# Kernel tuning notes

Hardware: AMD Instinct MI355X
Metric: run time of the kernel (lower is better)

Reference implementation:

```python
import jax, jax.numpy as jnp
import numpy as np

N, E, F = 50000, 400000, 128
H0, C0 = 1, 128   # layer 0: heads=1, out=128 (concat=False -> mean over heads)
H1, C1 = 4, 64    # layer 1: heads=4, out=64
EPS_BN = 1e-5
NEG_SLOPE = 0.2


def setup_inputs() -> dict:
    key = jax.random.key(0)
    ks = jax.random.split(key, 12)

    def w(k, shape, fan_in):
        return jax.random.normal(k, shape, jnp.float32) / np.float32(np.sqrt(fan_in))

    return {
        "emb": jax.random.normal(ks[0], (N, F), jnp.float32),
        "edge_weight": jax.random.uniform(ks[1], (E,), jnp.float32),
        # GATv2Conv layer 0 params (lin_l, lin_r, lin_edge, att, out bias)
        "Wl0": w(ks[2], (F, H0 * C0), F), "bl0": jnp.zeros((H0 * C0,), jnp.float32),
        "Wr0": w(ks[3], (F, H0 * C0), F), "br0": jnp.zeros((H0 * C0,), jnp.float32),
        "We0": w(ks[4], (1, H0 * C0), 1), "att0": w(ks[5], (H0, C0), C0),
        "b0": jnp.zeros((C0,), jnp.float32),
        "g0": jnp.ones((C0,), jnp.float32), "be0": jnp.zeros((C0,), jnp.float32),
        # GATv2Conv layer 1 params
        "Wl1": w(ks[6], (C0, H1 * C1), C0), "bl1": jnp.zeros((H1 * C1,), jnp.float32),
        "Wr1": w(ks[7], (C0, H1 * C1), C0), "br1": jnp.zeros((H1 * C1,), jnp.float32),
        "We1": w(ks[8], (1, H1 * C1), 1), "att1": w(ks[9], (H1, C1), C1),
        "b1": jnp.zeros((C1,), jnp.float32),
        "g1": jnp.ones((C1,), jnp.float32), "be1": jnp.zeros((C1,), jnp.float32),
        "edge_index": jax.random.randint(ks[10], (2, E), 0, N, jnp.int32),
    }


def gatv2(x, src, dst, ea, Wl, bl, Wr, br, We, att, b, H, C):
    """PyG GATv2Conv, edge_dim=1, concat=False (mean over heads), eval dropout."""
    n = x.shape[0]
    xl = (x @ Wl + bl).reshape(n, H, C)
    xr = (x @ Wr + br).reshape(n, H, C)
    ef = (ea[:, None] @ We).reshape(-1, H, C)           # [Et,H,C] edge embedding
    m = jax.nn.leaky_relu(xl[src] + xr[dst] + ef, NEG_SLOPE)  # [Et,H,C]
    alpha = jnp.einsum('ehc,hc->eh', m, att)            # attention logits
    amax = jax.ops.segment_max(alpha, dst, num_segments=n)
    ex = jnp.exp(alpha - amax[dst])
    den = jax.ops.segment_sum(ex, dst, num_segments=n)
    a = ex / (den[dst] + 1e-16)                          # segment softmax (PyG eps)
    out = jax.ops.segment_sum(a[:, :, None] * xl[src], dst, num_segments=n)
    return out.mean(axis=1) + b                          # concat=False -> head mean


def batchnorm(x, g, be):
    mu = x.mean(0)
    v = x.var(0)  # biased variance, as torch BN uses for normalization
    return g * (x - mu) * jax.lax.rsqrt(v + EPS_BN) + be


def _forward(emb, edge_weight, Wl0, bl0, Wr0, br0, We0, att0, b0, g0, be0,
             Wl1, bl1, Wr1, br1, We1, att1, b1, g1, be1, edge_index):
    loop = jnp.arange(N, dtype=edge_index.dtype)
    src = jnp.concatenate([edge_index[0], loop])
    dst = jnp.concatenate([edge_index[1], loop])
    # add_self_loops with fill_value='mean' for edge_attr
    ea = jnp.concatenate([edge_weight, jnp.full((N,), edge_weight.mean(), edge_weight.dtype)])
    # NOTE: zip(layer_stack, batchnorm_stack) truncates -> only first 2 of 3 GAT
    # layers execute, each followed by BN + ELU (+ identity dropout, p=0).
    h = gatv2(emb, src, dst, ea, Wl0, bl0, Wr0, br0, We0, att0, b0, H0, C0)
    h = jax.nn.elu(batchnorm(h, g0, be0))
    h = gatv2(h, src, dst, ea, Wl1, bl1, Wr1, br1, We1, att1, b1, H1, C1)
    h = jax.nn.elu(batchnorm(h, g1, be1))
    return h


def reference(emb, edge_weight, Wl0, bl0, Wr0, br0, We0, att0, b0, g0, be0,
              Wl1, bl1, Wr1, br1, We1, att1, b1, g1, be1, edge_index):
    return _forward(emb, edge_weight, Wl0, bl0, Wr0, br0, We0, att0, b0, g0, be0,
                    Wl1, bl1, Wr1, br1, We1, att1, b1, g1, be1, edge_index)
```

## Files before the change

### kernel.cpp

```cpp
#include <hip/hip_runtime.h>
#include <cstdint>
#include <cstddef>
#include <type_traits>

using f32x4 = __attribute__((ext_vector_type(4))) float;
using s16x8 = __attribute__((ext_vector_type(8))) short;

__device__ __forceinline__ ushort f2bf(float x) {
    uint32_t u = __builtin_bit_cast(uint32_t, x);
    u += 0x7fffu + ((u >> 16) & 1u);
    return (ushort)(u >> 16);
}
__device__ __forceinline__ float bflo(uint32_t u) { return __builtin_bit_cast(float, u << 16); }
__device__ __forceinline__ float bfhi(uint32_t u) { return __builtin_bit_cast(float, u & 0xffff0000u); }

__device__ __forceinline__ void dec8(uint4 g, float* x) {
    x[0] = bflo(g.x); x[1] = bfhi(g.x); x[2] = bflo(g.y); x[3] = bfhi(g.y);
    x[4] = bflo(g.z); x[5] = bfhi(g.z); x[6] = bflo(g.w); x[7] = bfhi(g.w);
}

#define GLOAD_LDS16(g, l)                                                                  \
    __builtin_amdgcn_global_load_lds((const __attribute__((address_space(1))) void*)(g),  \
                                     (__attribute__((address_space(3))) void*)(l), 16, 0, 0)

__global__ __launch_bounds__(256) void degree_ew_wt(const int* __restrict__ ei,
                                                    const float* __restrict__ ew,
                                                    int* __restrict__ deg,
                                                    float* __restrict__ partials,
                                                    int E, int N, int NBE,
                                                    const float* __restrict__ Wl0,
                                                    const float* __restrict__ Wr0,
                                                    ushort* __restrict__ WT0,
                                                    const float* __restrict__ Wl1,
                                                    const float* __restrict__ Wr1,
                                                    ushort* __restrict__ WT1) {
    __shared__ float red[256];
    int bid = blockIdx.x;
    int t = threadIdx.x;
    if (bid < NBE) {
        int e = bid * 256 + t;
        float s = (e < E) ? ew[e] : 0.f;
        red[t] = s; __syncthreads();
        for (int o = 128; o; o >>= 1) { if (t < o) red[t] += red[t + o]; __syncthreads(); }
        if (t == 0) partials[bid] = red[0];
        if (e < E + N) {
            int d = (e < E) ? ei[E + e] : (e - E);
            atomicAdd(&deg[d], 1);
        }
        return;
    }
    int j = (bid - NBE) * 256 + t;
    if (j < 128 * 256) {
        int k = j >> 8, c = j & 255;
        float v = (c < 128) ? Wl0[k * 128 + c] : Wr0[k * 128 + (c - 128)];
        WT0[(size_t)c * 128 + k] = f2bf(v);
        return;
    }
    j -= 128 * 256;
    if (j < 128 * 512) {
        int k = j >> 9, c = j & 511;
        float v = (c < 256) ? Wl1[k * 256 + c] : Wr1[k * 256 + (c - 256)];
        WT1[(size_t)c * 128 + k] = f2bf(v);
    }
}

__global__ void scan_partial(const int* __restrict__ deg, int n, int* __restrict__ bsum) {
    __shared__ int lds[256];
    int t = threadIdx.x;
    int base = blockIdx.x * 1024 + t * 4;
    int s = 0;
#pragma unroll
    for (int j = 0; j < 4; ++j) if (base + j < n) s += deg[base + j];
    lds[t] = s; __syncthreads();
    for (int o = 128; o; o >>= 1) { if (t < o) lds[t] += lds[t + o]; __syncthreads(); }
    if (t == 0) bsum[blockIdx.x] = lds[0];
}

__global__ void scan_block(const int* __restrict__ bsum, int nb, int* __restrict__ boff,
                           int* __restrict__ row_start, int n, int total,
                           const float* __restrict__ partials, int nbp, int E,
                           float* __restrict__ stats) {
    __shared__ int lds[256];
    __shared__ float fred[256];
    int t = threadIdx.x;
    int v = (t < nb) ? bsum[t] : 0;
    lds[t] = v; __syncthreads();
    for (int o = 1; o < 256; o <<= 1) {
        int y = (t >= o) ? lds[t - o] : 0;
        __syncthreads();
        lds[t] += y;
        __syncthreads();
    }
    if (t < nb) boff[t] = lds[t] - v;
    if (t == 0) row_start[n] = total;
    stats[t] = 0.f; stats[256 + t] = 0.f;
    float fs = 0.f;
    for (int j = t; j < nbp; j += 256) fs += partials[j];
    fred[t] = fs; __syncthreads();
    for (int o = 128; o; o >>= 1) { if (t < o) fred[t] += fred[t + o]; __syncthreads(); }
    if (t == 0) stats[0] = fred[0] / (float)E;
}

__global__ void scan_final(const int* __restrict__ deg, int n, const int* __restrict__ boff,
                           int* __restrict__ row_start, int* __restrict__ cursor) {
    __shared__ int lds[256];
    int t = threadIdx.x;
    int base = blockIdx.x * 1024 + t * 4;
    int d[4], loc[4], s = 0;
#pragma unroll
    for (int j = 0; j < 4; ++j) d[j] = (base + j < n) ? deg[base + j] : 0;
#pragma unroll
    for (int j = 0; j < 4; ++j) { loc[j] = s; s += d[j]; }
    lds[t] = s; __syncthreads();
    for (int o = 1; o < 256; o <<= 1) {
        int y = (t >= o) ? lds[t - o] : 0;
        __syncthreads();
        lds[t] += y;
        __syncthreads();
    }
    int texcl = lds[t] - s + boff[blockIdx.x];
#pragma unroll
    for (int j = 0; j < 4; ++j)
        if (base + j < n) { row_start[base + j] = texcl + loc[j]; cursor[base + j] = 0; }
}

__global__ void scatter_kernel(const int* __restrict__ ei, const float* __restrict__ ew,
                               const float* __restrict__ ew_mean, const int* __restrict__ row_start,
                               int* __restrict__ cursor, int* __restrict__ csr_src,
                               float* __restrict__ csr_ea, int E, int N) {
    int e = blockIdx.x * blockDim.x + threadIdx.x;
    if (e >= E + N) return;
    int s, d; float w;
    if (e < E) { s = ei[e]; d = ei[E + e]; w = ew[e]; }
    else       { s = d = e - E;            w = ew_mean[0]; }
    int pos = row_start[d] + atomicAdd(&cursor[d], 1);
    csr_src[pos] = s;
    csr_ea[pos] = w;
}

template <int MODE>
__global__ __launch_bounds__(512) void mfma_linear3(const void* __restrict__ Xv,
                                                    const ushort* __restrict__ WT,
                                                    const float* __restrict__ bnsums,
                                                    const float* __restrict__ gamma,
                                                    const float* __restrict__ beta,
                                                    const float* __restrict__ bl,
                                                    const float* __restrict__ br,
                                                    ushort* __restrict__ xl,
                                                    ushort* __restrict__ xr,
                                                    int n, int HALF) {
    constexpr int LW = (MODE == 1) ? 2 : 1;
    __shared__ ushort sB[128 * 128];
    __shared__ ushort sA[128 * 128];
    const int tid = threadIdx.x;
    const int c0 = blockIdx.x * 128;
    const int ntiles = (n + 127) >> 7;

    {
        const ushort* src = WT + (size_t)c0 * 128;
#pragma unroll
        for (int it = 0; it < 4; ++it) {
            int f = tid + it * 512;
            int row = f >> 4, ch = f & 15;
            const ushort* g = src + (size_t)row * 128 + ((ch ^ (row & 7)) << 3);
            ushort* lp = sB + (((size_t)it * 512 + (tid & ~63)) << 3);
            GLOAD_LDS16(g, lp);
        }
    }

    const int myc = (tid & 15) * 8;
    const int row0 = tid >> 4;
    const int swc = (tid & 15) ^ (row0 & 7);
    float Af[8], Bf[8];
    if constexpr (MODE == 2) {
        float invn = 1.f / (float)n;
#pragma unroll
        for (int j = 0; j < 8; ++j) {
            float mu = bnsums[myc + j] * invn;
            float var = bnsums[128 + myc + j] * invn - mu * mu;
            float rs = rsqrtf(var + 1e-5f);
            Af[j] = gamma[myc + j] * rs;
            Bf[j] = beta[myc + j] - mu * Af[j];
        }
    }

    uint4 rA[4][LW];
    auto loadA = [&](int rt) {
        int r0 = rt << 7;
#pragma unroll
        for (int it = 0; it < 4; ++it) {
            int gr = r0 + row0 + it * 32; gr = gr < n ? gr : n - 1;
            if constexpr (MODE == 1) {
                const float* src = (const float*)Xv + (size_t)gr * 128 + myc;
                rA[it][0] = *(const uint4*)src;
                rA[it][1] = *(const uint4*)(src + 4);
            } else {
                rA[it][0] = *(const uint4*)((const ushort*)Xv + (size_t)gr * 128 + myc);
            }
        }
    };
    auto writeA = [&]() {
#pragma unroll
        for (int it = 0; it < 4; ++it) {
            uint4 o;
            if constexpr (MODE == 0) {
                o = rA[it][0];
            } else if constexpr (MODE == 1) {
                float x[8] = {
                    __builtin_bit_cast(float, rA[it][0].x), __builtin_bit_cast(float, rA[it][0].y),
                    __builtin_bit_cast(float, rA[it][0].z), __builtin_bit_cast(float, rA[it][0].w),
                    __builtin_bit_cast(float, rA[it][1].x), __builtin_bit_cast(float, rA[it][1].y),
                    __builtin_bit_cast(float, rA[it][1].z), __builtin_bit_cast(float, rA[it][1].w)};
                ushort h[8];
#pragma unroll
                for (int j = 0; j < 8; ++j) h[j] = f2bf(x[j]);
                o.x = h[0] | ((uint32_t)h[1] << 16); o.y = h[2] | ((uint32_t)h[3] << 16);
                o.z = h[4] | ((uint32_t)h[5] << 16); o.w = h[6] | ((uint32_t)h[7] << 16);
            } else {
                float x[8]; dec8(rA[it][0], x);
                ushort h[8];
#pragma unroll
                for (int j = 0; j < 8; ++j) {
                    float v = fmaf(x[j], Af[j], Bf[j]);
                    v = v > 0.f ? v : __expf(v) - 1.f;
                    h[j] = f2bf(v);
                }
                o.x = h[0] | ((uint32_t)h[1] << 16); o.y = h[2] | ((uint32_t)h[3] << 16);
                o.z = h[4] | ((uint32_t)h[5] << 16); o.w = h[6] | ((uint32_t)h[7] << 16);
            }
            *(uint4*)&sA[(row0 + it * 32) * 128 + swc * 8] = o;
        }
    };

    const int w = tid >> 6, l = tid & 63, lr = l & 15, lg = l >> 4;
    const bool left = c0 < HALF;
    const float* bias = left ? bl : br;
    ushort* dst = left ? xl : xr;
    const int cb = left ? c0 : c0 - HALF;
    float bv[8];
#pragma unroll
    for (int tn = 0; tn < 8; ++tn) bv[tn] = bias[cb + tn * 16 + lr];
    const int arow = w * 16 + lr;

    int rt = blockIdx.y;
    loadA(rt);
    writeA();
    __syncthreads();

    while (true) {
        int nx = rt + gridDim.y;
        if (nx < ntiles) loadA(nx);

        f32x4 acc[8] = {};
#pragma unroll
        for (int kk = 0; kk < 4; ++kk) {
            int ach = (kk * 4 + lg) ^ (arow & 7);
            s16x8 a = *(const s16x8*)&sA[arow * 128 + (ach << 3)];
#pragma unroll
            for (int tn = 0; tn < 8; ++tn) {
                int brow = tn * 16 + lr;
                int bch = (kk * 4 + lg) ^ (brow & 7);
                s16x8 b = *(const s16x8*)&sB[brow * 128 + (bch << 3)];
                acc[tn] = __builtin_amdgcn_mfma_f32_16x16x32_bf16(a, b, acc[tn], 0, 0, 0);
            }
        }
        int rbase = (rt << 7) + w * 16 + lg * 4;
#pragma unroll
        for (int tn = 0; tn < 8; ++tn) {
            int colh = cb + tn * 16 + lr;
#pragma unroll
            for (int r = 0; r < 4; ++r) {
                int row = rbase + r;
                if (row < n) dst[(size_t)row * HALF + colh] = f2bf(acc[tn][r] + bv[tn]);
            }
        }
        if (nx >= ntiles) break;
        __syncthreads();
        writeA();
        __syncthreads();
        rt = nx;
    }
}

template <int H, int C, int LPN>
__global__ __launch_bounds__(256, 8) void gat_agg(const ushort* __restrict__ xl,
                                                  const ushort* __restrict__ xr,
                                                  const int* __restrict__ row_start,
                                                  const int* __restrict__ csr_src,
                                                  const float* __restrict__ csr_ea,
                                                  const float* __restrict__ We,
                                                  const float* __restrict__ att,
                                                  const float* __restrict__ bias,
                                                  ushort* __restrict__ out, int n) {
    constexpr int HC = H * C;
    constexpr int VPL = HC / LPN;
    constexpr int REDW = LPN / H;
    constexpr int NPW = 64 / LPN;
    static_assert(VPL == 8, "");

    const int wid = threadIdx.x >> 6;
    const int lane = threadIdx.x & 63;
    const int sl = lane & (LPN - 1);
    const int sub = lane / LPN;
    const int v = (blockIdx.x * 4 + wid) * NPW + sub;
    const bool valid = v < n;
    const int vv = valid ? v : n - 1;

    const int base = sl * VPL;
    const int e0 = row_start[vv];
    const int e1 = valid ? row_start[vv + 1] : row_start[vv + 1];

    uint4 gN; float wN;
    {
        int s = csr_src[e0];
        wN = csr_ea[e0];
        gN = *(const uint4*)&xl[(size_t)s * HC + base];
    }

    float xrv[8], wE[8], attv[8];
    dec8(*(const uint4*)&xr[(size_t)vv * HC + base], xrv);
#pragma unroll
    for (int j = 0; j < 8; j += 4) {
        float4 a = *(const float4*)&We[base + j];
        wE[j] = a.x; wE[j + 1] = a.y; wE[j + 2] = a.z; wE[j + 3] = a.w;
        float4 b = *(const float4*)&att[base + j];
        attv[j] = b.x; attv[j + 1] = b.y; attv[j + 2] = b.z; attv[j + 3] = b.w;
    }

    float m, den, acc[8];
    {
        uint4 g = gN; float w = wN;
        if (e0 + 1 < e1) {
            int s = csr_src[e0 + 1];
            wN = csr_ea[e0 + 1];
            gN = *(const uint4*)&xl[(size_t)s * HC + base];
        }
        float xf[8];
        dec8(g, xf);
        float t1 = 0.f, t2 = 0.f;
#pragma unroll
        for (int j = 0; j < 8; ++j) {
            float u = xf[j] + fmaf(w, wE[j], xrv[j]);
            t1 = fmaf(u, attv[j], t1);
            t2 = fmaf(__builtin_fabsf(u), attv[j], t2);
        }
        float p = fmaf(0.6f, t1, 0.4f * t2);
#pragma unroll
        for (int o = REDW >> 1; o; o >>= 1) p += __shfl_xor(p, o, 64);
        m = p; den = 1.f;
#pragma unroll
        for (int j = 0; j < 8; ++j) acc[j] = xf[j];
    }

    for (int e = e0 + 1; e < e1; ++e) {
        uint4 g = gN; float w = wN;
        if (e + 1 < e1) {
            int s = csr_src[e + 1];
            wN = csr_ea[e + 1];
            gN = *(const uint4*)&xl[(size_t)s * HC + base];
        }
        float xf[8];
        dec8(g, xf);
        float t1 = 0.f, t2 = 0.f;
#pragma unroll
        for (int j = 0; j < 8; ++j) {
            float u = xf[j] + fmaf(w, wE[j], xrv[j]);
            t1 = fmaf(u, attv[j], t1);
            t2 = fmaf(__builtin_fabsf(u), attv[j], t2);
        }
        float p = fmaf(0.6f, t1, 0.4f * t2);
#pragma unroll
        for (int o = REDW >> 1; o; o >>= 1) p += __shfl_xor(p, o, 64);
        float dd = p - m;
        if (__builtin_expect(dd > 8.f, 0)) {
            float r = __expf(-dd);
            den = fmaf(den, r, 1.f);
#pragma unroll
            for (int j = 0; j < 8; ++j) acc[j] = fmaf(acc[j], r, xf[j]);
            m = p;
        } else {
            float pe = __expf(dd);
            den += pe;
#pragma unroll
            for (int j = 0; j < 8; ++j) acc[j] = fmaf(pe, xf[j], acc[j]);
        }
    }

    float inv = 1.f / den;
#pragma unroll
    for (int j = 0; j < 8; ++j) acc[j] *= inv;

    if constexpr (H > 1) {
#pragma unroll
        for (int o = REDW; o < LPN; o <<= 1)
#pragma unroll
            for (int j = 0; j < 8; ++j) acc[j] += __shfl_xor(acc[j], o, 64);
#pragma unroll
        for (int j = 0; j < 8; ++j) acc[j] *= (1.f / (float)H);
    }

    if (valid && sl < C / VPL) {
        float bv[8];
#pragma unroll
        for (int j = 0; j < 8; j += 4) {
            float4 b = *(const float4*)&bias[sl * VPL + j];
            bv[j] = b.x; bv[j + 1] = b.y; bv[j + 2] = b.z; bv[j + 3] = b.w;
        }
        uint4 o;
        o.x = (uint32_t)f2bf(acc[0] + bv[0]) | ((uint32_t)f2bf(acc[1] + bv[1]) << 16);
        o.y = (uint32_t)f2bf(acc[2] + bv[2]) | ((uint32_t)f2bf(acc[3] + bv[3]) << 16);
        o.z = (uint32_t)f2bf(acc[4] + bv[4]) | ((uint32_t)f2bf(acc[5] + bv[5]) << 16);
        o.w = (uint32_t)f2bf(acc[6] + bv[6]) | ((uint32_t)f2bf(acc[7] + bv[7]) << 16);
        *(uint4*)&out[(size_t)v * C + sl * VPL] = o;
    }
}

template <int C>
__global__ __launch_bounds__(256) void bn_stats_bf16(const ushort* __restrict__ x, int n,
                                                     float* __restrict__ sums) {
    constexpr int C2 = C / 2;
    constexpr int RPB = 256 / C2;
    __shared__ float red[256];
    int t = threadIdx.x;
    int c2 = t % C2, rs = t / C2;
    float s0 = 0.f, s1 = 0.f, q0 = 0.f, q1 = 0.f;
    for (int row = blockIdx.x * RPB + rs; row < n; row += gridDim.x * RPB) {
        uint32_t u = *(const uint32_t*)&x[(size_t)row * C + c2 * 2];
        float a = bflo(u), b = bfhi(u);
        s0 += a; q0 += a * a; s1 += b; q1 += b * b;
    }
    float vals[4] = {s0, s1, q0, q1};
    float outv[4];
#pragma unroll
    for (int k = 0; k < 4; ++k) {
        red[t] = vals[k]; __syncthreads();
        if (rs == 0) {
            float s = red[c2];
#pragma unroll
            for (int r = 1; r < RPB; ++r) s += red[c2 + r * C2];
            outv[k] = s;
        }
        __syncthreads();
    }
    if (rs == 0) {
        atomicAdd(&sums[c2 * 2],     outv[0]);
        atomicAdd(&sums[c2 * 2 + 1], outv[1]);
        atomicAdd(&sums[C + c2 * 2],     outv[2]);
        atomicAdd(&sums[C + c2 * 2 + 1], outv[3]);
    }
}

template <int C>
__global__ __launch_bounds__(256) void bn_apply_elu_f32(const ushort* __restrict__ x, int n,
                                                        const float* __restrict__ g,
                                                        const float* __restrict__ be,
                                                        const float* __restrict__ sums,
                                                        float* __restrict__ outf) {
    int total = n * C / 8;
    float invn = 1.f / (float)n;
    for (int i = blockIdx.x * blockDim.x + threadIdx.x; i < total; i += gridDim.x * blockDim.x) {
        uint4 u = ((const uint4*)x)[i];
        int c0 = (i * 8) & (C - 1);
        float r[8] = {bflo(u.x), bfhi(u.x), bflo(u.y), bfhi(u.y),
                      bflo(u.z), bfhi(u.z), bflo(u.w), bfhi(u.w)};
#pragma unroll
        for (int j = 0; j < 8; ++j) {
            int c = c0 + j;
            float mu = sums[c] * invn;
            float var = sums[C + c] * invn - mu * mu;
            float t = g[c] * (r[j] - mu) * rsqrtf(var + 1e-5f) + be[c];
            r[j] = t > 0.f ? t : expm1f(t);
        }
        ((float4*)outf)[i * 2]     = make_float4(r[0], r[1], r[2], r[3]);
        ((float4*)outf)[i * 2 + 1] = make_float4(r[4], r[5], r[6], r[7]);
    }
}

extern "C" void kernel_launch(void* const* d_in, const int* in_sizes, int n_in,
                              void* d_out, int out_size, void* d_ws, size_t ws_size,
                              hipStream_t stream) {
    const float* emb = (const float*)d_in[0];
    const float* ew  = (const float*)d_in[1];
    const float* Wl0 = (const float*)d_in[2];
    const float* bl0 = (const float*)d_in[3];
    const float* Wr0 = (const float*)d_in[4];
    const float* br0 = (const float*)d_in[5];
    const float* We0 = (const float*)d_in[6];
    const float* att0 = (const float*)d_in[7];
    const float* b0  = (const float*)d_in[8];
    const float* g0  = (const float*)d_in[9];
    const float* be0 = (const float*)d_in[10];
    const float* Wl1 = (const float*)d_in[11];
    const float* bl1 = (const float*)d_in[12];
    const float* Wr1 = (const float*)d_in[13];
    const float* br1 = (const float*)d_in[14];
    const float* We1 = (const float*)d_in[15];
    const float* att1 = (const float*)d_in[16];
    const float* b1  = (const float*)d_in[17];
    const float* g1  = (const float*)d_in[18];
    const float* be1 = (const float*)d_in[19];
    const int* ei    = (const int*)d_in[20];

    const int N = in_sizes[0] / 128;
    const int E = in_sizes[1];
    const int Et = E + N;
    float* out = (float*)d_out;

    char* w = (char*)d_ws;
    size_t off = 0;
    auto alloc = [&](size_t bytes) {
        void* p = w + off;
        off = (off + bytes + 255) & ~(size_t)255;
        return p;
    };
    ushort* xlb    = (ushort*)alloc((size_t)N * 256 * 2);
    ushort* xrb    = (ushort*)alloc((size_t)N * 256 * 2);
    ushort* h0b16  = (ushort*)alloc((size_t)N * 128 * 2);
    ushort* out16  = (ushort*)alloc((size_t)N * 64 * 2);
    ushort* WT0    = (ushort*)alloc((size_t)256 * 128 * 2);
    ushort* WT1    = (ushort*)alloc((size_t)512 * 128 * 2);
    int*   deg     = (int*)alloc((size_t)2 * N * 4);
    int*   cursor  = deg + N;
    int*   row_st  = (int*)alloc((size_t)(N + 1) * 4);
    int*   csr_src = (int*)alloc((size_t)Et * 4);
    float* csr_ea  = (float*)alloc((size_t)Et * 4);
    int*   bsum    = (int*)alloc(256 * 4);
    int*   boff    = (int*)alloc(256 * 4);
    float* partials= (float*)alloc(2048 * 4);
    float* stats   = (float*)alloc(512 * 4);
    float* ew_mean = stats;
    float* bn0     = stats + 64;
    float* bn1     = stats + 64 + 256;
    (void)ws_size; (void)n_in; (void)out_size;

    hipMemsetAsync(deg, 0, (size_t)N * 4, stream);

    const int NBE = (Et + 255) / 256;
    const int WTB = (128 * 256 + 128 * 512) / 256;
    degree_ew_wt<<<NBE + WTB, 256, 0, stream>>>(ei, ew, deg, partials, E, N, NBE,
                                                Wl0, Wr0, WT0, Wl1, Wr1, WT1);
    const int NB1 = (N + 1023) / 1024;
    scan_partial<<<NB1, 256, 0, stream>>>(deg, N, bsum);
    scan_block<<<1, 256, 0, stream>>>(bsum, NB1, boff, row_st, N, Et, partials, NBE, E, stats);
    scan_final<<<NB1, 256, 0, stream>>>(deg, N, boff, row_st, cursor);
    scatter_kernel<<<NBE, 256, 0, stream>>>(ei, ew, ew_mean, row_st, cursor,
                                            csr_src, csr_ea, E, N);

    const int ntiles = (N + 127) / 128;
    const int GR0 = ntiles < 128 ? ntiles : 128;
    const int GR1 = ntiles < 64 ? ntiles : 64;

    mfma_linear3<1><<<dim3(2, GR0), 512, 0, stream>>>(emb, WT0, nullptr, nullptr, nullptr,
                                                      bl0, br0, xlb, xrb, N, 128);
    gat_agg<1, 128, 16><<<(N + 15) / 16, 256, 0, stream>>>(xlb, xrb, row_st, csr_src, csr_ea,
                                                           We0, att0, b0, h0b16, N);
    bn_stats_bf16<128><<<128, 256, 0, stream>>>(h0b16, N, bn0);

    mfma_linear3<2><<<dim3(4, GR1), 512, 0, stream>>>(h0b16, WT1, bn0, g0, be0,
                                                      bl1, br1, xlb, xrb, N, 256);
    gat_agg<4, 64, 32><<<(N + 7) / 8, 256, 0, stream>>>(xlb, xrb, row_st, csr_src, csr_ea,
                                                        We1, att1, b1, out16, N);
    bn_stats_bf16<64><<<128, 256, 0, stream>>>(out16, N, bn1);
    bn_apply_elu_f32<64><<<1024, 256, 0, stream>>>(out16, N, g1, be1, bn1, out);
}
```

Before: 267.7 us.

## Unroll GAT aggregation by two edges with deeper prefetch and raise GEMM grid

The edge loop in gat_agg now handles two edges per iteration. It prefetches the next two neighbour rows, computes both logits together, and does one online-softmax rescale against their max. The aim is to keep more gather loads in flight and cut the serial dependency per edge. Launch bounds drop to 6 waves to leave room for the extra registers, which may lower occupancy. The linear GEMM grids grow to up to 256 row tiles, with an early return for surplus blocks.

```diff
diff --git a/kernel.cpp b/kernel.cpp
--- a/kernel.cpp
+++ b/kernel.cpp
@@ -243,6 +243,7 @@
     const int arow = w * 16 + lr;
 
     int rt = blockIdx.y;
+    if (rt >= ntiles) return;
     loadA(rt);
     writeA();
     __syncthreads();
@@ -283,7 +284,7 @@
 }
 
 template <int H, int C, int LPN>
-__global__ __launch_bounds__(256, 8) void gat_agg(const ushort* __restrict__ xl,
+__global__ __launch_bounds__(256, 6) void gat_agg(const ushort* __restrict__ xl,
                                                   const ushort* __restrict__ xr,
                                                   const int* __restrict__ row_start,
                                                   const int* __restrict__ csr_src,
@@ -308,13 +309,23 @@
 
     const int base = sl * VPL;
     const int e0 = row_start[vv];
-    const int e1 = valid ? row_start[vv + 1] : row_start[vv + 1];
-
-    uint4 gN; float wN;
+    const int e1 = row_start[vv + 1];
+    const ushort* xlb = xl + base;
+
+    uint4 gF; float wF;
     {
         int s = csr_src[e0];
-        wN = csr_ea[e0];
-        gN = *(const uint4*)&xl[(size_t)s * HC + base];
+        wF = csr_ea[e0];
+        gF = *(const uint4*)&xlb[(size_t)s * HC];
+    }
+    uint4 gA, gB; float wA, wB;
+    {
+        int ea = e0 + 1 < e1 ? e0 + 1 : e0;
+        int eb = e0 + 2 < e1 ? e0 + 2 : e0;
+        int sa = csr_src[ea]; wA = csr_ea[ea];
+        int sb = csr_src[eb]; wB = csr_ea[eb];
+        gA = *(const uint4*)&xlb[(size_t)sa * HC];
+        gB = *(const uint4*)&xlb[(size_t)sb * HC];
     }
 
     float xrv[8], wE[8], attv[8];
@@ -329,18 +340,12 @@
 
     float m, den, acc[8];
     {
-        uint4 g = gN; float w = wN;
-        if (e0 + 1 < e1) {
-            int s = csr_src[e0 + 1];
-            wN = csr_ea[e0 + 1];
-            gN = *(const uint4*)&xl[(size_t)s * HC + base];
-        }
         float xf[8];
-        dec8(g, xf);
+        dec8(gF, xf);
         float t1 = 0.f, t2 = 0.f;
 #pragma unroll
         for (int j = 0; j < 8; ++j) {
-            float u = xf[j] + fmaf(w, wE[j], xrv[j]);
+            float u = xf[j] + fmaf(wF, wE[j], xrv[j]);
             t1 = fmaf(u, attv[j], t1);
             t2 = fmaf(__builtin_fabsf(u), attv[j], t2);
         }
@@ -352,19 +357,59 @@
         for (int j = 0; j < 8; ++j) acc[j] = xf[j];
     }
 
-    for (int e = e0 + 1; e < e1; ++e) {
-        uint4 g = gN; float w = wN;
-        if (e + 1 < e1) {
-            int s = csr_src[e + 1];
-            wN = csr_ea[e + 1];
-            gN = *(const uint4*)&xl[(size_t)s * HC + base];
-        }
+    int e = e0 + 1;
+    while (e + 1 < e1) {
+        uint4 g0 = gA, g1 = gB; float w0 = wA, w1 = wB;
+        {
+            int ea = e + 2 < e1 ? e + 2 : e;
+            int eb = e + 3 < e1 ? e + 3 : e;
+            int sa = csr_src[ea]; wA = csr_ea[ea];
+            int sb = csr_src[eb]; wB = csr_ea[eb];
+            gA = *(const uint4*)&xlb[(size_t)sa * HC];
+            gB = *(const uint4*)&xlb[(size_t)sb * HC];
+        }
+        float xf0[8], xf1[8];
+        dec8(g0, xf0); dec8(g1, xf1);
+        float t10 = 0.f, t20 = 0.f, t11 = 0.f, t21 = 0.f;
+#pragma unroll
+        for (int j = 0; j < 8; ++j) {
+            float u0 = xf0[j] + fmaf(w0, wE[j], xrv[j]);
+            float u1 = xf1[j] + fmaf(w1, wE[j], xrv[j]);
+            t10 = fmaf(u0, attv[j], t10);
+            t20 = fmaf(__builtin_fabsf(u0), attv[j], t20);
+            t11 = fmaf(u1, attv[j], t11);
+            t21 = fmaf(__builtin_fabsf(u1), attv[j], t21);
+        }
+        float p0 = fmaf(0.6f, t10, 0.4f * t20);
+        float p1 = fmaf(0.6f, t11, 0.4f * t21);
+#pragma unroll
+        for (int o = REDW >> 1; o; o >>= 1) {
+            p0 += __shfl_xor(p0, o, 64);
+            p1 += __shfl_xor(p1, o, 64);
+        }
+        float pm = fmaxf(p0, p1);
+        if (__builtin_expect(pm - m > 8.f, 0)) {
+            float r = __expf(m - pm);
+            den *= r;
+#pragma unroll
+            for (int j = 0; j < 8; ++j) acc[j] *= r;
+            m = pm;
+        }
+        float pe0 = __expf(p0 - m);
+        float pe1 = __expf(p1 - m);
+        den += pe0 + pe1;
+#pragma unroll
+        for (int j = 0; j < 8; ++j)
+            acc[j] = fmaf(pe1, xf1[j], fmaf(pe0, xf0[j], acc[j]));
+        e += 2;
+    }
+    if (e < e1) {
         float xf[8];
-        dec8(g, xf);
+        dec8(gA, xf);
         float t1 = 0.f, t2 = 0.f;
 #pragma unroll
         for (int j = 0; j < 8; ++j) {
-            float u = xf[j] + fmaf(w, wE[j], xrv[j]);
+            float u = xf[j] + fmaf(wA, wE[j], xrv[j]);
             t1 = fmaf(u, attv[j], t1);
             t2 = fmaf(__builtin_fabsf(u), attv[j], t2);
         }
@@ -547,17 +592,16 @@
                                             csr_src, csr_ea, E, N);
 
     const int ntiles = (N + 127) / 128;
-    const int GR0 = ntiles < 128 ? ntiles : 128;
-    const int GR1 = ntiles < 64 ? ntiles : 64;
-
-    mfma_linear3<1><<<dim3(2, GR0), 512, 0, stream>>>(emb, WT0, nullptr, nullptr, nullptr,
-                                                      bl0, br0, xlb, xrb, N, 128);
+    const int GR = ntiles < 256 ? ntiles : 256;
+
+    mfma_linear3<1><<<dim3(2, GR), 512, 0, stream>>>(emb, WT0, nullptr, nullptr, nullptr,
+                                                     bl0, br0, xlb, xrb, N, 128);
     gat_agg<1, 128, 16><<<(N + 15) / 16, 256, 0, stream>>>(xlb, xrb, row_st, csr_src, csr_ea,
                                                            We0, att0, b0, h0b16, N);
     bn_stats_bf16<128><<<128, 256, 0, stream>>>(h0b16, N, bn0);
 
-    mfma_linear3<2><<<dim3(4, GR1), 512, 0, stream>>>(h0b16, WT1, bn0, g0, be0,
-                                                      bl1, br1, xlb, xrb, N, 256);
+    mfma_linear3<2><<<dim3(4, GR), 512, 0, stream>>>(h0b16, WT1, bn0, g0, be0,
+                                                     bl1, br1, xlb, xrb, N, 256);
     gat_agg<4, 64, 32><<<(N + 7) / 8, 256, 0, stream>>>(xlb, xrb, row_st, csr_src, csr_ea,
                                                         We1, att1, b1, out16, N);
     bn_stats_bf16<64><<<128, 256, 0, stream>>>(out16, N, bn1);
```

Measured after the change: 254.8 us. -4.8%, faster.
